# Kernel tuning notes

Measured on AMD Instinct MI355X. Metric: run time of the kernel, lower is better.

The kernel has to match this reference:

```python
import jax, jax.numpy as jnp
from jax import lax
import numpy as np

H = 32  # hidden_size


def setup_inputs() -> dict:
    key = jax.random.key(0)
    ks = jax.random.split(key, 12)
    B, T, I = 4096, 1024, 1
    s = lambda fan_in: 1.0 / np.sqrt(fan_in)
    inp = {
        "x": jax.random.normal(ks[0], (B, I, T), dtype=jnp.float32),
        # LSTM params, PyTorch layout: gates stacked as [i, f, g, o]
        "W_ih": jax.random.uniform(ks[1], (4 * H, I), jnp.float32, -s(H), s(H)),
        "W_hh": jax.random.uniform(ks[2], (4 * H, H), jnp.float32, -s(H), s(H)),
        "b_ih": jax.random.uniform(ks[3], (4 * H,), jnp.float32, -s(H), s(H)),
        "b_hh": jax.random.uniform(ks[4], (4 * H,), jnp.float32, -s(H), s(H)),
        # MLP head: 32 -> 16 -> 8 -> 1
        "W1": jax.random.uniform(ks[5], (16, H), jnp.float32, -s(H), s(H)),
        "b1": jax.random.uniform(ks[6], (16,), jnp.float32, -s(H), s(H)),
        "W2": jax.random.uniform(ks[7], (8, 16), jnp.float32, -s(16), s(16)),
        "b2": jax.random.uniform(ks[8], (8,), jnp.float32, -s(16), s(16)),
        "W3": jax.random.uniform(ks[9], (1, 8), jnp.float32, -s(8), s(8)),
        "b3": jax.random.uniform(ks[10], (1,), jnp.float32, -s(8), s(8)),
    }
    return inp


def reference(x, W_ih, W_hh, b_ih, b_hh, W1, b1, W2, b2, W3, b3):
    # x: (B, 1, T) -> (B, T, 1), batch_first LSTM over T
    xs = jnp.transpose(x, (0, 2, 1))
    B, T, _ = xs.shape
    # Precompute input contribution to all gates: (B, T, 4H)
    xW = jnp.einsum('bti,gi->btg', xs, W_ih) + (b_ih + b_hh)

    def step(carry, xw_t):
        h, c = carry
        gates = xw_t + h @ W_hh.T  # (B, 4H)
        i, f, g, o = jnp.split(gates, 4, axis=-1)
        c = jax.nn.sigmoid(f) * c + jax.nn.sigmoid(i) * jnp.tanh(g)
        h = jax.nn.sigmoid(o) * jnp.tanh(c)
        return (h, c), None

    h0 = jnp.zeros((B, H), xs.dtype)
    (h_n, _), _ = lax.scan(step, (h0, h0), jnp.swapaxes(xW, 0, 1))

    # MLP head on final hidden state h_n[-1] (single layer -> h_n itself)
    out = jax.nn.relu(h_n @ W1.T + b1)
    out = jax.nn.relu(out @ W2.T + b2)
    return out @ W3.T + b3  # (B, 1)
```

## Files before the change

### kernel.cpp

```cpp
#include <hip/hip_runtime.h>

#define HSZ 32
#define TT  1024

typedef float v2f __attribute__((ext_vector_type(2)));

__device__ __forceinline__ float frcp(float x) { return __builtin_amdgcn_rcpf(x); }
__device__ __forceinline__ float sigm(float z) { return frcp(1.0f + __expf(-z)); }
__device__ __forceinline__ float tanh_(float z) {
  return fmaf(2.0f, frcp(1.0f + __expf(-2.0f * z)), -1.0f);
}

__global__ __launch_bounds__(256, 2)
void lstm_fused_kernel(const float* __restrict__ x,
                       const float* __restrict__ W_ih,
                       const float* __restrict__ W_hh,
                       const float* __restrict__ b_ih,
                       const float* __restrict__ b_hh,
                       const float* __restrict__ W1, const float* __restrict__ b1,
                       const float* __restrict__ W2, const float* __restrict__ b2,
                       const float* __restrict__ W3, const float* __restrict__ b3,
                       float* __restrict__ out)
{
  __shared__ __align__(16) float hlds[8][HSZ];

  const int tid  = threadIdx.x;
  const int wave = tid >> 6;
  const int lane = tid & 63;
  const int grp  = lane >> 5;
  const int j    = lane & 31;
  const int we   = wave * 2 + grp;
  const int elem = blockIdx.x * 8 + we;

  v2f w0[16], w1[16], w2[16], w3[16];
  {
    const float4* r0 = reinterpret_cast<const float4*>(W_hh + (0 * 32 + j) * HSZ);
    const float4* r1 = reinterpret_cast<const float4*>(W_hh + (1 * 32 + j) * HSZ);
    const float4* r2 = reinterpret_cast<const float4*>(W_hh + (2 * 32 + j) * HSZ);
    const float4* r3 = reinterpret_cast<const float4*>(W_hh + (3 * 32 + j) * HSZ);
#pragma unroll
    for (int k4 = 0; k4 < 8; ++k4) {
      float4 a = r0[k4]; w0[2*k4] = (v2f){a.x, a.y}; w0[2*k4+1] = (v2f){a.z, a.w};
      float4 b = r1[k4]; w1[2*k4] = (v2f){b.x, b.y}; w1[2*k4+1] = (v2f){b.z, b.w};
      float4 c = r2[k4]; w2[2*k4] = (v2f){c.x, c.y}; w2[2*k4+1] = (v2f){c.z, c.w};
      float4 d = r3[k4]; w3[2*k4] = (v2f){d.x, d.y}; w3[2*k4+1] = (v2f){d.z, d.w};
    }
  }
#pragma unroll
  for (int k = 0; k < 16; ++k) {
    asm volatile("" : "+v"(w0[k]), "+v"(w1[k]), "+v"(w2[k]), "+v"(w3[k]));
  }

  const float bi0 = b_ih[0 * 32 + j] + b_hh[0 * 32 + j];
  const float bi1 = b_ih[1 * 32 + j] + b_hh[1 * 32 + j];
  const float bi2 = b_ih[2 * 32 + j] + b_hh[2 * 32 + j];
  const float bi3 = b_ih[3 * 32 + j] + b_hh[3 * 32 + j];
  const float wx0 = W_ih[0 * 32 + j];
  const float wx1 = W_ih[1 * 32 + j];
  const float wx2 = W_ih[2 * 32 + j];
  const float wx3 = W_ih[3 * 32 + j];

  v2f h2[16];
#pragma unroll
  for (int k = 0; k < 16; ++k) h2[k] = (v2f){0.0f, 0.0f};
  float c = 0.0f;

  const float* xrow = x + (size_t)elem * TT;

#pragma unroll 1
  for (int t0 = 0; t0 < TT; t0 += 32) {
    float xc = xrow[t0 + j];
#pragma unroll 1
    for (int s = 0; s < 32; ++s) {
      float xt = __shfl(xc, s, 32);

      v2f acc0 = (v2f){bi0, 0.0f};
      v2f acc1 = (v2f){bi1, 0.0f};
      v2f acc2 = (v2f){bi2, 0.0f};
      v2f acc3 = (v2f){bi3, 0.0f};
#pragma unroll
      for (int k = 0; k < 16; ++k) {
        acc0 = __builtin_elementwise_fma(w0[k], h2[k], acc0);
        acc1 = __builtin_elementwise_fma(w1[k], h2[k], acc1);
        acc2 = __builtin_elementwise_fma(w2[k], h2[k], acc2);
        acc3 = __builtin_elementwise_fma(w3[k], h2[k], acc3);
      }
      float a0 = acc0.x + fmaf(xt, wx0, acc0.y);
      float a1 = acc1.x + fmaf(xt, wx1, acc1.y);
      float a2 = acc2.x + fmaf(xt, wx2, acc2.y);
      float a3 = acc3.x + fmaf(xt, wx3, acc3.y);

      float si = sigm(a0), sf = sigm(a1), tg = tanh_(a2), so = sigm(a3);
      c = fmaf(sf, c, si * tg);
      float hj = so * tanh_(c);

      hlds[we][j] = hj;
#pragma unroll
      for (int k4 = 0; k4 < 8; ++k4) {
        float4 v = *reinterpret_cast<const float4*>(&hlds[we][4 * k4]);
        h2[2*k4]   = (v2f){v.x, v.y};
        h2[2*k4+1] = (v2f){v.z, v.w};
      }
    }
  }

  const float* hrow = &hlds[we][0];
  float a1v[16];
#pragma unroll
  for (int r = 0; r < 16; ++r) {
    float acc = b1[r];
#pragma unroll
    for (int k = 0; k < 32; ++k) acc = fmaf(W1[r * 32 + k], hrow[k], acc);
    a1v[r] = fmaxf(acc, 0.0f);
  }
  float a2v[8];
#pragma unroll
  for (int r = 0; r < 8; ++r) {
    float acc = b2[r];
#pragma unroll
    for (int k = 0; k < 16; ++k) acc = fmaf(W2[r * 16 + k], a1v[k], acc);
    a2v[r] = fmaxf(acc, 0.0f);
  }
  float o = b3[0];
#pragma unroll
  for (int k = 0; k < 8; ++k) o = fmaf(W3[k], a2v[k], o);

  if (j == 0) out[elem] = o;
}

extern "C" void kernel_launch(void* const* d_in, const int* in_sizes, int n_in,
                              void* d_out, int out_size, void* d_ws, size_t ws_size,
                              hipStream_t stream) {
  const float* x    = (const float*)d_in[0];
  const float* W_ih = (const float*)d_in[1];
  const float* W_hh = (const float*)d_in[2];
  const float* b_ih = (const float*)d_in[3];
  const float* b_hh = (const float*)d_in[4];
  const float* W1   = (const float*)d_in[5];
  const float* b1   = (const float*)d_in[6];
  const float* W2   = (const float*)d_in[7];
  const float* b2   = (const float*)d_in[8];
  const float* W3   = (const float*)d_in[9];
  const float* b3   = (const float*)d_in[10];
  float* out = (float*)d_out;

  const int B = in_sizes[0] / TT;
  dim3 grid(B / 8), block(256);
  hipLaunchKernelGGL(lstm_fused_kernel, grid, block, 0, stream,
                     x, W_ih, W_hh, b_ih, b_hh, W1, b1, W2, b2, W3, b3, out);
}
```

Baseline: 491.9 us.

## Split LSTM gates across wave halves, one batch element per wave

Each 64-lane wave now handles a single batch element. Each half-wave computes two of the four gates (i,f on one half, g,o on the other) and the halves trade results with a cross-half shuffle, so each lane does half the matvec FMAs and half the weight registers. Gate weights, biases and input weights are prescaled by -log2e (or -2log2e for tanh) so activations use a raw exp2 plus reciprocal. This doubles the number of waves and adds a shuffle per step. Lanes of the second half write an unused LDS row, and there is no barrier between the h write and read, which relies on the single wave running in lockstep.

```diff
diff --git a/kernel.cpp b/kernel.cpp
--- a/kernel.cpp
+++ b/kernel.cpp
@@ -2,16 +2,15 @@
 
 #define HSZ 32
 #define TT  1024
+#define LOG2E 1.44269504088896340736f
 
 typedef float v2f __attribute__((ext_vector_type(2)));
+typedef float v4f __attribute__((ext_vector_type(4)));
 
-__device__ __forceinline__ float frcp(float x) { return __builtin_amdgcn_rcpf(x); }
-__device__ __forceinline__ float sigm(float z) { return frcp(1.0f + __expf(-z)); }
-__device__ __forceinline__ float tanh_(float z) {
-  return fmaf(2.0f, frcp(1.0f + __expf(-2.0f * z)), -1.0f);
-}
+__device__ __forceinline__ float frcp(float x)  { return __builtin_amdgcn_rcpf(x); }
+__device__ __forceinline__ float fexp2(float x) { return __builtin_amdgcn_exp2f(x); }
 
-__global__ __launch_bounds__(256, 2)
+__global__ __launch_bounds__(64, 4)
 void lstm_fused_kernel(const float* __restrict__ x,
                        const float* __restrict__ W_ih,
                        const float* __restrict__ W_hh,
@@ -22,43 +21,36 @@
                        const float* __restrict__ W3, const float* __restrict__ b3,
                        float* __restrict__ out)
 {
-  __shared__ __align__(16) float hlds[8][HSZ];
+  __shared__ __align__(16) float hlds[2][HSZ];
 
-  const int tid  = threadIdx.x;
-  const int wave = tid >> 6;
-  const int lane = tid & 63;
-  const int grp  = lane >> 5;
+  const int lane = threadIdx.x;
+  const int half = lane >> 5;
   const int j    = lane & 31;
-  const int we   = wave * 2 + grp;
-  const int elem = blockIdx.x * 8 + we;
+  const int elem = blockIdx.x;
 
-  v2f w0[16], w1[16], w2[16], w3[16];
+  const int r1 = (half ? 2 : 0) * HSZ + j;
+  const int r2 = (half ? 3 : 1) * HSZ + j;
+  const float s1 = half ? (-2.0f * LOG2E) : (-LOG2E);
+  const float s2 = -LOG2E;
+  const float A1 = half ? 2.0f : 1.0f;
+  const float B1 = half ? -1.0f : 0.0f;
+
+  v2f w1[16], w2[16];
   {
-    const float4* r0 = reinterpret_cast<const float4*>(W_hh + (0 * 32 + j) * HSZ);
-    const float4* r1 = reinterpret_cast<const float4*>(W_hh + (1 * 32 + j) * HSZ);
-    const float4* r2 = reinterpret_cast<const float4*>(W_hh + (2 * 32 + j) * HSZ);
-    const float4* r3 = reinterpret_cast<const float4*>(W_hh + (3 * 32 + j) * HSZ);
+    const v4f* p1 = reinterpret_cast<const v4f*>(W_hh + r1 * HSZ);
+    const v4f* p2 = reinterpret_cast<const v4f*>(W_hh + r2 * HSZ);
 #pragma unroll
     for (int k4 = 0; k4 < 8; ++k4) {
-      float4 a = r0[k4]; w0[2*k4] = (v2f){a.x, a.y}; w0[2*k4+1] = (v2f){a.z, a.w};
-      float4 b = r1[k4]; w1[2*k4] = (v2f){b.x, b.y}; w1[2*k4+1] = (v2f){b.z, b.w};
-      float4 c = r2[k4]; w2[2*k4] = (v2f){c.x, c.y}; w2[2*k4+1] = (v2f){c.z, c.w};
-      float4 d = r3[k4]; w3[2*k4] = (v2f){d.x, d.y}; w3[2*k4+1] = (v2f){d.z, d.w};
+      v4f a = p1[k4] * s1;
+      v4f b = p2[k4] * s2;
+      w1[2*k4] = a.lo; w1[2*k4+1] = a.hi;
+      w2[2*k4] = b.lo; w2[2*k4+1] = b.hi;
     }
   }
-#pragma unroll
-  for (int k = 0; k < 16; ++k) {
-    asm volatile("" : "+v"(w0[k]), "+v"(w1[k]), "+v"(w2[k]), "+v"(w3[k]));
-  }
-
-  const float bi0 = b_ih[0 * 32 + j] + b_hh[0 * 32 + j];
-  const float bi1 = b_ih[1 * 32 + j] + b_hh[1 * 32 + j];
-  const float bi2 = b_ih[2 * 32 + j] + b_hh[2 * 32 + j];
-  const float bi3 = b_ih[3 * 32 + j] + b_hh[3 * 32 + j];
-  const float wx0 = W_ih[0 * 32 + j];
-  const float wx1 = W_ih[1 * 32 + j];
-  const float wx2 = W_ih[2 * 32 + j];
-  const float wx3 = W_ih[3 * 32 + j];
+  const float bz1  = s1 * (b_ih[r1] + b_hh[r1]);
+  const float bz2  = s2 * (b_ih[r2] + b_hh[r2]);
+  const float wxz1 = s1 * W_ih[r1];
+  const float wxz2 = s2 * W_ih[r2];
 
   v2f h2[16];
 #pragma unroll
@@ -68,43 +60,50 @@
   const float* xrow = x + (size_t)elem * TT;
 
 #pragma unroll 1
-  for (int t0 = 0; t0 < TT; t0 += 32) {
-    float xc = xrow[t0 + j];
+  for (int t0 = 0; t0 < TT; t0 += 64) {
+    float xc = xrow[t0 + lane];
+
+#pragma unroll
+    for (int k = 0; k < 16; k += 4) {
+      asm volatile("" : "+v"(w1[k]), "+v"(w1[k+1]), "+v"(w1[k+2]), "+v"(w1[k+3]),
+                        "+v"(w2[k]), "+v"(w2[k+1]), "+v"(w2[k+2]), "+v"(w2[k+3]));
+    }
+
 #pragma unroll 1
-    for (int s = 0; s < 32; ++s) {
-      float xt = __shfl(xc, s, 32);
+    for (int s = 0; s < 64; ++s) {
+      float xt = __shfl(xc, s);
 
-      v2f acc0 = (v2f){bi0, 0.0f};
-      v2f acc1 = (v2f){bi1, 0.0f};
-      v2f acc2 = (v2f){bi2, 0.0f};
-      v2f acc3 = (v2f){bi3, 0.0f};
+      v2f a1 = (v2f){bz1, 0.0f};
+      v2f a2 = (v2f){bz2, 0.0f};
 #pragma unroll
       for (int k = 0; k < 16; ++k) {
-        acc0 = __builtin_elementwise_fma(w0[k], h2[k], acc0);
-        acc1 = __builtin_elementwise_fma(w1[k], h2[k], acc1);
-        acc2 = __builtin_elementwise_fma(w2[k], h2[k], acc2);
-        acc3 = __builtin_elementwise_fma(w3[k], h2[k], acc3);
+        a1 = __builtin_elementwise_fma(w1[k], h2[k], a1);
+        a2 = __builtin_elementwise_fma(w2[k], h2[k], a2);
       }
-      float a0 = acc0.x + fmaf(xt, wx0, acc0.y);
-      float a1 = acc1.x + fmaf(xt, wx1, acc1.y);
-      float a2 = acc2.x + fmaf(xt, wx2, acc2.y);
-      float a3 = acc3.x + fmaf(xt, wx3, acc3.y);
+      float z1 = a1.x + fmaf(xt, wxz1, a1.y);
+      float z2 = a2.x + fmaf(xt, wxz2, a2.y);
 
-      float si = sigm(a0), sf = sigm(a1), tg = tanh_(a2), so = sigm(a3);
-      c = fmaf(sf, c, si * tg);
-      float hj = so * tanh_(c);
+      float act1 = fmaf(A1, frcp(1.0f + fexp2(z1)), B1);
+      float act2 = frcp(1.0f + fexp2(z2));
 
-      hlds[we][j] = hj;
+      float tg = __shfl_xor(act1, 32);
+      float so = __shfl_xor(act2, 32);
+
+      c = fmaf(act2, c, act1 * tg);
+      float tc = fmaf(2.0f, frcp(1.0f + fexp2(c * (-2.0f * LOG2E))), -1.0f);
+      float h = so * tc;
+
+      hlds[half][j] = h;
 #pragma unroll
       for (int k4 = 0; k4 < 8; ++k4) {
-        float4 v = *reinterpret_cast<const float4*>(&hlds[we][4 * k4]);
-        h2[2*k4]   = (v2f){v.x, v.y};
-        h2[2*k4+1] = (v2f){v.z, v.w};
+        v4f v = *reinterpret_cast<const v4f*>(&hlds[0][4 * k4]);
+        h2[2*k4]   = v.lo;
+        h2[2*k4+1] = v.hi;
       }
     }
   }
 
-  const float* hrow = &hlds[we][0];
+  const float* hrow = &hlds[0][0];
   float a1v[16];
 #pragma unroll
   for (int r = 0; r < 16; ++r) {
@@ -125,7 +124,7 @@
 #pragma unroll
   for (int k = 0; k < 8; ++k) o = fmaf(W3[k], a2v[k], o);
 
-  if (j == 0) out[elem] = o;
+  if (lane == 0) out[elem] = o;
 }
 
 extern "C" void kernel_launch(void* const* d_in, const int* in_sizes, int n_in,
@@ -145,7 +144,7 @@
   float* out = (float*)d_out;
 
   const int B = in_sizes[0] / TT;
-  dim3 grid(B / 8), block(256);
+  dim3 grid(B), block(64);
   hipLaunchKernelGGL(lstm_fused_kernel, grid, block, 0, stream,
                      x, W_ih, W_hh, b_ih, b_hh, W1, b1, W2, b2, W3, b3, out);
 }
```

Result: slower. 580.6 us (+18.0%).
